# Optimization experiments

Measured on AMD Instinct MI355X. Metric: run time of the kernel, lower is better.

## Reference

```python
import jax, jax.numpy as jnp
import numpy as np

VOCAB = 50257
SEQ = 2048
EMB = 512
BATCH = 8


def setup_inputs() -> dict:
    key = jax.random.key(0)
    k1, k2, k3 = jax.random.split(key, 3)
    tokens = jax.random.randint(k1, (BATCH, SEQ), 0, VOCAB, dtype=jnp.int64 if jax.config.jax_enable_x64 else jnp.int32)
    W_emb = jax.random.normal(k2, (EMB, VOCAB), dtype=jnp.float32)
    W_pos = jax.random.normal(k3, (SEQ, EMB), dtype=jnp.float32)
    return {"tokens": tokens, "W_emb": W_emb, "W_pos": W_pos}


def reference(tokens, W_emb, W_pos):
    # Original: one_hot(tokens, V).float() @ W_emb.T  -> identical to gathering
    # columns of W_emb, i.e. rows of W_emb.T. Shapes: (B,S) -> (B,S,E)
    tok_emb = jnp.take(W_emb.T, tokens, axis=0)  # (B, S, E)
    # positional weight (S, E) broadcasts over batch
    return tok_emb + W_pos
```

## Files before the change

kernel.cpp:

```cpp
#include <hip/hip_runtime.h>

#define VOCAB 50257
#define SEQ   2048
#define EMB   512
#define BATCH 8

constexpr int TILE = 32;

__global__ __launch_bounds__(256)
void transpose_k(const float* __restrict__ in, float* __restrict__ out) {
    __shared__ float tile[TILE][TILE + 1];
    const int v0 = blockIdx.x * TILE;
    const int e0 = blockIdx.y * TILE;
    const int tx = threadIdx.x;
    const int ty = threadIdx.y;

    const int v = v0 + tx;
    if (v < VOCAB) {
#pragma unroll
        for (int j = 0; j < TILE; j += 8) {
            tile[ty + j][tx] = in[(size_t)(e0 + ty + j) * VOCAB + v];
        }
    }
    __syncthreads();

    const int e = e0 + tx;
#pragma unroll
    for (int j = 0; j < TILE; j += 8) {
        const int vv = v0 + ty + j;
        if (vv < VOCAB) {
            out[(size_t)vv * EMB + e] = tile[tx][ty + j];
        }
    }
}

__device__ __forceinline__ float4 f4add(float4 a, float4 b) {
    return make_float4(a.x + b.x, a.y + b.y, a.z + b.z, a.w + b.w);
}

__global__ __launch_bounds__(256)
void gather_k(const int* __restrict__ tokens,
              const float4* __restrict__ WT,
              const float4* __restrict__ Wpos,
              float4* __restrict__ out) {
    const int idx = blockIdx.x * blockDim.x + threadIdx.x;
    const int e4  = idx & (EMB / 4 - 1);
    const int ts  = idx >> 7;
    const int s   = ts & (SEQ - 1);
    const int t   = tokens[ts];
    const float4 emb = WT[(size_t)t * (EMB / 4) + e4];
    const float4 pos = Wpos[(size_t)s * (EMB / 4) + e4];
    out[idx] = f4add(emb, pos);
}

__global__ __launch_bounds__(256)
void gather_direct_k(const int* __restrict__ tokens,
                     const float* __restrict__ W_emb,
                     const float4* __restrict__ Wpos,
                     float4* __restrict__ out) {
    const int idx = blockIdx.x * blockDim.x + threadIdx.x;
    const int e4  = idx & (EMB / 4 - 1);
    const int ts  = idx >> 7;
    const int s   = ts & (SEQ - 1);
    const int t   = tokens[ts];
    const int e   = e4 * 4;
    float4 r;
    r.x = W_emb[(size_t)(e + 0) * VOCAB + t];
    r.y = W_emb[(size_t)(e + 1) * VOCAB + t];
    r.z = W_emb[(size_t)(e + 2) * VOCAB + t];
    r.w = W_emb[(size_t)(e + 3) * VOCAB + t];
    out[idx] = f4add(r, Wpos[(size_t)s * (EMB / 4) + e4]);
}

extern "C" void kernel_launch(void* const* d_in, const int* in_sizes, int n_in,
                              void* d_out, int out_size, void* d_ws, size_t ws_size,
                              hipStream_t stream) {
    const int*   tokens = (const int*)d_in[0];
    const float* W_emb  = (const float*)d_in[1];
    const float* W_pos  = (const float*)d_in[2];
    float*       out    = (float*)d_out;

    const size_t need = (size_t)VOCAB * EMB * sizeof(float);
    const int n_out4  = BATCH * SEQ * (EMB / 4);
    const int gblocks = n_out4 / 256;

    if (ws_size >= need) {
        float* WT = (float*)d_ws;
        dim3 tgrid((VOCAB + TILE - 1) / TILE, EMB / TILE);
        transpose_k<<<tgrid, dim3(32, 8), 0, stream>>>(W_emb, WT);
        gather_k<<<gblocks, 256, 0, stream>>>(tokens, (const float4*)WT,
                                              (const float4*)W_pos, (float4*)out);
    } else {
        gather_direct_k<<<gblocks, 256, 0, stream>>>(tokens, W_emb,
                                                     (const float4*)W_pos, (float4*)out);
    }
}
```

Measured before the change: 192.1 us.

## Drop full-table transpose; gather strided columns directly with nontemporal stores

Removes the transpose of the whole embedding table into workspace, which moved about 100MB each call, and always uses the direct strided gather from W_emb. Output writes become nontemporal stores. The cost is uncoalesced scalar loads: each thread reads four elements spaced VOCAB apart, and threads in a wave hit random token columns, so most loads touch a separate cache line. Only 16K tokens are gathered, so the total bytes read are far fewer than the transpose moved.

```diff
diff --git a/kernel.cpp b/kernel.cpp
--- a/kernel.cpp
+++ b/kernel.cpp
@@ -5,71 +5,29 @@
 #define EMB   512
 #define BATCH 8
 
-constexpr int TILE = 32;
+typedef float floatx4 __attribute__((ext_vector_type(4)));
 
 __global__ __launch_bounds__(256)
-void transpose_k(const float* __restrict__ in, float* __restrict__ out) {
-    __shared__ float tile[TILE][TILE + 1];
-    const int v0 = blockIdx.x * TILE;
-    const int e0 = blockIdx.y * TILE;
-    const int tx = threadIdx.x;
-    const int ty = threadIdx.y;
-
-    const int v = v0 + tx;
-    if (v < VOCAB) {
-#pragma unroll
-        for (int j = 0; j < TILE; j += 8) {
-            tile[ty + j][tx] = in[(size_t)(e0 + ty + j) * VOCAB + v];
-        }
-    }
-    __syncthreads();
-
-    const int e = e0 + tx;
-#pragma unroll
-    for (int j = 0; j < TILE; j += 8) {
-        const int vv = v0 + ty + j;
-        if (vv < VOCAB) {
-            out[(size_t)vv * EMB + e] = tile[tx][ty + j];
-        }
-    }
-}
-
-__device__ __forceinline__ float4 f4add(float4 a, float4 b) {
-    return make_float4(a.x + b.x, a.y + b.y, a.z + b.z, a.w + b.w);
-}
-
-__global__ __launch_bounds__(256)
-void gather_k(const int* __restrict__ tokens,
-              const float4* __restrict__ WT,
-              const float4* __restrict__ Wpos,
-              float4* __restrict__ out) {
+void fused_gather_k(const int* __restrict__ tokens,
+                    const float* __restrict__ W_emb,
+                    const floatx4* __restrict__ Wpos,
+                    floatx4* __restrict__ out) {
     const int idx = blockIdx.x * blockDim.x + threadIdx.x;
     const int e4  = idx & (EMB / 4 - 1);
     const int ts  = idx >> 7;
     const int s   = ts & (SEQ - 1);
     const int t   = tokens[ts];
-    const float4 emb = WT[(size_t)t * (EMB / 4) + e4];
-    const float4 pos = Wpos[(size_t)s * (EMB / 4) + e4];
-    out[idx] = f4add(emb, pos);
-}
 
-__global__ __launch_bounds__(256)
-void gather_direct_k(const int* __restrict__ tokens,
-                     const float* __restrict__ W_emb,
-                     const float4* __restrict__ Wpos,
-                     float4* __restrict__ out) {
-    const int idx = blockIdx.x * blockDim.x + threadIdx.x;
-    const int e4  = idx & (EMB / 4 - 1);
-    const int ts  = idx >> 7;
-    const int s   = ts & (SEQ - 1);
-    const int t   = tokens[ts];
-    const int e   = e4 * 4;
-    float4 r;
-    r.x = W_emb[(size_t)(e + 0) * VOCAB + t];
-    r.y = W_emb[(size_t)(e + 1) * VOCAB + t];
-    r.z = W_emb[(size_t)(e + 2) * VOCAB + t];
-    r.w = W_emb[(size_t)(e + 3) * VOCAB + t];
-    out[idx] = f4add(r, Wpos[(size_t)s * (EMB / 4) + e4]);
+    const size_t base = (size_t)(4 * e4) * VOCAB + (size_t)t;
+    floatx4 r;
+    r.x = W_emb[base];
+    r.y = W_emb[base + (size_t)VOCAB];
+    r.z = W_emb[base + (size_t)(2 * VOCAB)];
+    r.w = W_emb[base + (size_t)(3 * VOCAB)];
+
+    const floatx4 p = Wpos[(size_t)s * (EMB / 4) + e4];
+    const floatx4 o = r + p;
+    __builtin_nontemporal_store(o, &out[idx]);
 }
 
 extern "C" void kernel_launch(void* const* d_in, const int* in_sizes, int n_in,
@@ -80,18 +38,10 @@
     const float* W_pos  = (const float*)d_in[2];
     float*       out    = (float*)d_out;
 
-    const size_t need = (size_t)VOCAB * EMB * sizeof(float);
     const int n_out4  = BATCH * SEQ * (EMB / 4);
     const int gblocks = n_out4 / 256;
 
-    if (ws_size >= need) {
-        float* WT = (float*)d_ws;
-        dim3 tgrid((VOCAB + TILE - 1) / TILE, EMB / TILE);
-        transpose_k<<<tgrid, dim3(32, 8), 0, stream>>>(W_emb, WT);
-        gather_k<<<gblocks, 256, 0, stream>>>(tokens, (const float4*)WT,
-                                              (const float4*)W_pos, (float4*)out);
-    } else {
-        gather_direct_k<<<gblocks, 256, 0, stream>>>(tokens, W_emb,
-                                                     (const float4*)W_pos, (float4*)out);
-    }
+    fused_gather_k<<<gblocks, 256, 0, stream>>>(tokens, W_emb,
+                                                (const floatx4*)W_pos,
+                                                (floatx4*)out);
 }
```

Result: slower. 289.1 us (+50.5%).
